# Optimization experiments

Measured on AMD Instinct MI355X. Metric: run time of the kernel, lower is better.

The kernel has to match this reference:

```python
import jax, jax.numpy as jnp
import numpy as np

NPOINT, RADIUS, NSAMPLE = 512, 0.2, 32
MLP = [64, 64, 128]
IN_CH = 67
EPS = 1e-5


def farthest_point_sample(xyz, npoint):
    # xyz: [B, N, 3] -> idx [B, npoint]. Deterministic start at index 0.
    B, N, _ = xyz.shape

    def step(carry, _):
        dist, far = carry  # dist [B,N], far [B]
        centroid = jnp.take_along_axis(xyz, far[:, None, None], axis=1)  # [B,1,3]
        d = jnp.sum((xyz - centroid) ** 2, axis=-1)  # [B,N]
        dist = jnp.minimum(dist, d)
        return (dist, jnp.argmax(dist, axis=-1).astype(jnp.int32)), far

    init = (jnp.full((B, N), 1e10, dtype=xyz.dtype), jnp.zeros((B,), jnp.int32))
    _, idxs = jax.lax.scan(step, init, None, length=npoint)
    return idxs.T  # [B, npoint]


def query_ball_point(radius, nsample, xyz, new_xyz):
    # xyz [B,N,3], new_xyz [B,S,3] -> idx [B,S,nsample]
    B, N, _ = xyz.shape
    sqr = jnp.sum((new_xyz[:, :, None, :] - xyz[:, None, :, :]) ** 2, axis=-1)  # [B,S,N]
    gidx = jnp.where(sqr > radius * radius, N, jnp.arange(N, dtype=jnp.int32))
    gidx = jnp.sort(gidx, axis=-1)[:, :, :nsample]
    first = gidx[:, :, :1]
    return jnp.where(gidx == N, first, gidx).astype(jnp.int32)


def gather_points(pts, idx):
    # pts [B,N,C], idx [B,...] -> [B,...,C]
    return jax.vmap(lambda p, i: p[i])(pts, idx)


def sample_and_group(npoint, radius, nsample, xyz, points):
    fps_idx = farthest_point_sample(xyz, npoint)          # [B,S]
    new_xyz = gather_points(xyz, fps_idx)                 # [B,S,3]
    idx = query_ball_point(radius, nsample, xyz, new_xyz)  # [B,S,K]
    grouped_xyz = gather_points(xyz, idx)                 # [B,S,K,3]
    grouped_xyz_norm = grouped_xyz - new_xyz[:, :, None, :]
    grouped_pts = gather_points(points, idx)              # [B,S,K,D]
    new_points = jnp.concatenate([grouped_xyz_norm, grouped_pts], axis=-1)  # [B,S,K,3+D]
    return new_xyz, new_points


def mlp_bn_relu(x, w, b, gamma, beta):
    # x [B,C,K,S]; 1x1 conv + training-mode BatchNorm2d + ReLU
    y = jnp.einsum('oc,bcks->boks', w, x) + b[None, :, None, None]
    mean = jnp.mean(y, axis=(0, 2, 3), keepdims=True)
    var = jnp.var(y, axis=(0, 2, 3), keepdims=True)
    y = (y - mean) * jax.lax.rsqrt(var + EPS)
    y = y * gamma[None, :, None, None] + beta[None, :, None, None]
    return jax.nn.relu(y)


def setup_inputs() -> dict:
    key = jax.random.key(0)
    ks = jax.random.split(key, 8)
    B, N, D = 16, 2048, 64
    inp = {
        'xyz': jax.random.normal(ks[0], (B, 3, N), jnp.float32),
        'points': jax.random.normal(ks[1], (B, D, N), jnp.float32),
    }
    last = IN_CH
    for i, out in enumerate(MLP):
        kw = jax.random.fold_in(ks[2], i)
        inp[f'w{i}'] = jax.random.normal(kw, (out, last), jnp.float32) * 0.05
        inp[f'b{i}'] = jnp.zeros((out,), jnp.float32)
        inp[f'g{i}'] = jnp.ones((out,), jnp.float32)
        inp[f'bt{i}'] = jnp.zeros((out,), jnp.float32)
        last = out
    return inp


def reference(xyz, points, w0, b0, g0, bt0, w1, b1, g1, bt1, w2, b2, g2, bt2):
    # xyz [B,3,N], points [B,D,N]
    xyz_t = jnp.transpose(xyz, (0, 2, 1))      # [B,N,3]
    pts_t = jnp.transpose(points, (0, 2, 1))   # [B,N,D]
    new_xyz, new_points = sample_and_group(NPOINT, RADIUS, NSAMPLE, xyz_t, pts_t)
    # [B,S,K,C] -> [B,C,K,S]
    x = jnp.transpose(new_points, (0, 3, 2, 1))
    for (w, b, g, bt) in ((w0, b0, g0, bt0), (w1, b1, g1, bt1), (w2, b2, g2, bt2)):
        x = mlp_bn_relu(x, w, b, g, bt)
    feature = jnp.max(x, axis=2)               # [B,C',S]
    new_xyz_out = jnp.transpose(new_xyz, (0, 2, 1))  # [B,3,S]
    return new_xyz_out, feature
```

## Files before the change

kernel.cpp:

```cpp
#include <hip/hip_runtime.h>
#include <hip/hip_bf16.h>
#include <stdint.h>

#define NB 16
#define NPT 2048
#define NS 512
#define NK 32
#define PTOT (NB*NS*NK)
#define C_IN 67
#define EPSV 1e-5f

typedef __attribute__((ext_vector_type(8))) short short8;
typedef __attribute__((ext_vector_type(4))) float floatx4;

#define WS_NEWXYZ 0
#define WS_ST     24576
#define WS_W1BF   27136
#define WS_W2BF   29184
#define WS_RAWMAX 33280
#define WS_PTS_TB 557568
#define WS_Y1     1606144
#define WS_Y2     9994752

__device__ __forceinline__ float bf2f(ushort u){ return __uint_as_float((uint32_t)u<<16); }
__device__ __forceinline__ ushort f2bf(float f){
  uint32_t u = __float_as_uint(f);
  return (ushort)((u + 0x7FFFu + ((u>>16)&1u)) >> 16);
}

template<int CTRL>
__device__ __forceinline__ double dppmax64f(double k){
  long long b = __double_as_longlong(k);
  int lo = (int)(uint32_t)b, hi = (int)(b>>32);
  int olo = __builtin_amdgcn_update_dpp(lo, lo, CTRL, 0xF, 0xF, false);
  int ohi = __builtin_amdgcn_update_dpp(hi, hi, CTRL, 0xF, 0xF, false);
  double o = __hiloint2double(ohi, olo);
  return fmax(o, k);
}
__device__ __forceinline__ unsigned long long u64max(unsigned long long a, unsigned long long b){ return a>b?a:b; }

__global__ __launch_bounds__(256) void prep_kernel(const float* __restrict__ xyz,
    float* __restrict__ nxyz, float* __restrict__ out0,
    const float* __restrict__ pts, ushort* __restrict__ pts_tb,
    const float* __restrict__ w1, const float* __restrict__ w2,
    ushort* __restrict__ w1b, ushort* __restrict__ w2b, float* __restrict__ st)
{
  __shared__ union {
    struct { float4 lc[NPT]; double warr[2][4]; int sel[NS]; } f;
    float tile[64][65];
  } sm;
  const int blk = blockIdx.x;
  const int tid = threadIdx.x;
  if (blk < 16){
    const int b = blk;
    const float* xb = xyz + (size_t)b*3*NPT;
    float px[8], py[8], pz[8], dist[8];
    uint32_t lo_[8];
    #pragma unroll
    for (int j=0;j<8;j++){
      int n = j*256 + tid;
      float x = xb[n], y = xb[NPT+n], z = xb[2*NPT+n];
      sm.f.lc[n] = make_float4(x,y,z,0.f);
      px[j]=x; py[j]=y; pz[j]=z; dist[j]=1e10f;
      lo_[j] = ~(uint32_t)n;
    }
    if (tid==0) sm.f.sel[0]=0;
    __syncthreads();
    float4 c0 = sm.f.lc[0];
    float cx = c0.x, cy = c0.y, cz = c0.z;
    const int lane = tid & 63, wid = tid >> 6;
    for (int t=1;t<NS;t++){
      double kk[8];
      #pragma unroll
      for (int j=0;j<8;j++){
        float dx = __fsub_rn(px[j], cx);
        float dy = __fsub_rn(py[j], cy);
        float dz = __fsub_rn(pz[j], cz);
        float d  = __fadd_rn(__fadd_rn(__fmul_rn(dx,dx),__fmul_rn(dy,dy)),__fmul_rn(dz,dz));
        float dd = fminf(dist[j], d);
        dist[j] = dd;
        kk[j] = __hiloint2double((int)__float_as_uint(dd), (int)lo_[j]);
      }
      double m0 = fmax(kk[0],kk[1]), m1 = fmax(kk[2],kk[3]);
      double m2 = fmax(kk[4],kk[5]), m3 = fmax(kk[6],kk[7]);
      double best = fmax(fmax(m0,m1), fmax(m2,m3));
      best = dppmax64f<0xB1>(best);
      best = dppmax64f<0x4E>(best);
      best = dppmax64f<0x124>(best);
      best = dppmax64f<0x128>(best);
      long long bb = __double_as_longlong(best);
      int bl = (int)(uint32_t)bb, bh = (int)(bb>>32);
      unsigned long long k0 = (((unsigned long long)(uint32_t)__builtin_amdgcn_readlane(bh, 0))<<32)  | (uint32_t)__builtin_amdgcn_readlane(bl, 0);
      unsigned long long k1 = (((unsigned long long)(uint32_t)__builtin_amdgcn_readlane(bh, 16))<<32) | (uint32_t)__builtin_amdgcn_readlane(bl, 16);
      unsigned long long k2 = (((unsigned long long)(uint32_t)__builtin_amdgcn_readlane(bh, 32))<<32) | (uint32_t)__builtin_amdgcn_readlane(bl, 32);
      unsigned long long k3 = (((unsigned long long)(uint32_t)__builtin_amdgcn_readlane(bh, 48))<<32) | (uint32_t)__builtin_amdgcn_readlane(bl, 48);
      unsigned long long kw = u64max(u64max(k0,k1), u64max(k2,k3));
      if (lane==0) sm.f.warr[t&1][wid] = __longlong_as_double((long long)kw);
      __syncthreads();
      double w0 = sm.f.warr[t&1][0], w1_ = sm.f.warr[t&1][1], w2_ = sm.f.warr[t&1][2], w3 = sm.f.warr[t&1][3];
      double f = fmax(fmax(w0,w1_), fmax(w2_,w3));
      int n = (int)(~(uint32_t)__double_as_longlong(f));
      float4 cc = sm.f.lc[n];
      cx = cc.x; cy = cc.y; cz = cc.z;
      if (tid==0) sm.f.sel[t]=n;
    }
    __syncthreads();
    for (int s = tid; s < NS; s += 256){
      int n = sm.f.sel[s];
      float4 cc = sm.f.lc[n];
      float* np_ = nxyz + ((size_t)b*NS + s)*3;
      np_[0]=cc.x; np_[1]=cc.y; np_[2]=cc.z;
      float* ob = out0 + (size_t)b*3*NS + s;
      ob[0]=cc.x; ob[NS]=cc.y; ob[2*NS]=cc.z;
    }
  } else if (blk < 528){
    const int t2 = blk - 16;
    const int b = t2 >> 5;
    const int n0 = (t2 & 31) * 64;
    const int lane = tid & 63;
    const int row4 = tid >> 6;
    const float* src = pts + (size_t)b*64*NPT;
    #pragma unroll
    for (int r=0; r<16; r++){
      int cc = r*4 + row4;
      sm.tile[cc][lane] = src[(size_t)cc*NPT + n0 + lane];
    }
    __syncthreads();
    ushort* dst = pts_tb + ((size_t)b*NPT + n0)*64;
    #pragma unroll
    for (int r=0; r<16; r++){
      int nn = r*4 + row4;
      dst[(size_t)nn*64 + lane] = f2bf(sm.tile[lane][nn]);
    }
  } else {
    for (int i = tid; i < 4096; i += 256) w1b[i] = f2bf(w1[i]);
    for (int i = tid; i < 8192; i += 256) w2b[i] = f2bf(w2[i]);
    for (int i = tid; i < 2560; i += 256) st[i] = 0.f;
  }
}

__global__ __launch_bounds__(256) void conv1_kernel(const float* __restrict__ xyz,
    const ushort* __restrict__ pts_tb, const float* __restrict__ nxyz,
    const float* __restrict__ Wt, const float* __restrict__ bias,
    ushort* __restrict__ y1)
{
  __shared__ int gq[8][NK];
  const int tid = threadIdx.x;
  const int wid = tid>>6, lane = tid&63;
  const int p0 = blockIdx.x*256;
  const int bs0 = p0 >> 5;
  const int b = p0 >> 14;
  const float* xb = xyz + (size_t)b*3*NPT;
  const float r2 = 0.2f*0.2f;
  for (int gi=0; gi<2; gi++){
    const int gl = wid*2 + gi;
    const float* c = nxyz + (size_t)(bs0+gl)*3;
    const float cx = c[0], cy = c[1], cz = c[2];
    int cnt = 0, first = 0;
    for (int ch=0; ch<NPT/64 && cnt<NK; ch++){
      int n = ch*64 + lane;
      float dx = __fsub_rn(cx, xb[n]);
      float dy = __fsub_rn(cy, xb[NPT+n]);
      float dz = __fsub_rn(cz, xb[2*NPT+n]);
      float d  = __fadd_rn(__fadd_rn(__fmul_rn(dx,dx),__fmul_rn(dy,dy)),__fmul_rn(dz,dz));
      bool in = (d <= r2);
      unsigned long long mask = __ballot(in);
      if (mask){
        if (cnt==0) first = ch*64 + (__ffsll((unsigned long long)mask)-1);
        if (in){
          int pos = cnt + __popcll(mask & ((1ull<<lane)-1ull));
          if (pos < NK) gq[gl][pos] = n;
        }
        cnt += __popcll(mask);
      }
    }
    if (cnt < NK && lane >= cnt && lane < NK) gq[gl][lane] = first;
  }
  __syncthreads();
  const int p = p0 + tid;
  const int bs = p >> 5;
  const int n = gq[tid>>5][tid&31];
  float x[C_IN];
  {
    const float* cc = nxyz + (size_t)bs*3;
    x[0] = xb[n]        - cc[0];
    x[1] = xb[NPT+n]    - cc[1];
    x[2] = xb[2*NPT+n]  - cc[2];
    const ushort* pr = pts_tb + ((size_t)b*NPT + n)*64;
    #pragma unroll
    for (int q=0;q<8;q++){
      short8 v = *(const short8*)(pr + q*8);
      #pragma unroll
      for (int j=0;j<8;j++) x[3+8*q+j] = bf2f((ushort)v[j]);
    }
  }
  ushort* yr = y1 + (size_t)p*64;
  #pragma unroll 1
  for (int o=0;o<64;o+=8){
    float a[8];
    #pragma unroll
    for (int k=0;k<8;k++) a[k] = bias[o+k];
    #pragma unroll
    for (int c=0;c<C_IN;c++){
      float xv = x[c];
      #pragma unroll
      for (int k=0;k<8;k++) a[k] = fmaf(Wt[(o+k)*C_IN+c], xv, a[k]);
    }
    short8 sv;
    #pragma unroll
    for (int k=0;k<8;k++) sv[k] = (short)f2bf(a[k]);
    *(short8*)(yr + o) = sv;
  }
}

__global__ __launch_bounds__(256) void stats64_kernel(const ushort* __restrict__ y,
                                                      float* __restrict__ stbase)
{
  const int wid = threadIdx.x>>6, lane = threadIdx.x&63;
  const int oct = lane & 7, pr = lane >> 3;
  const int p0 = blockIdx.x*1024 + wid*256;
  float s[8], s2[8];
  #pragma unroll
  for (int j=0;j<8;j++){ s[j]=0.f; s2[j]=0.f; }
  for (int it=0; it<32; it++){
    int p = p0 + it*8 + pr;
    short8 v = *(const short8*)(y + (size_t)p*64 + oct*8);
    #pragma unroll
    for (int j=0;j<8;j++){
      float f = bf2f((ushort)v[j]);
      s[j] += f; s2[j] = fmaf(f,f,s2[j]);
    }
  }
  #pragma unroll
  for (int off=8; off<64; off<<=1){
    #pragma unroll
    for (int j=0;j<8;j++){ s[j] += __shfl_xor(s[j],off,64); s2[j] += __shfl_xor(s2[j],off,64); }
  }
  __shared__ float sd[4][128];
  if (pr==0){
    #pragma unroll
    for (int j=0;j<8;j++){ sd[wid][oct*8+j] = s[j]; sd[wid][64+oct*8+j] = s2[j]; }
  }
  __syncthreads();
  int t = threadIdx.x;
  if (t < 128){
    float v = sd[0][t]+sd[1][t]+sd[2][t]+sd[3][t];
    int rep = blockIdx.x & 1;
    float* dst = (t<64) ? (stbase + rep*64 + t) : (stbase + 128 + rep*64 + (t-64));
    atomicAdd(dst, v);
  }
}

__global__ __launch_bounds__(256) void conv2_mfma(const ushort* __restrict__ yin,
    const float* __restrict__ st, const float* __restrict__ g0, const float* __restrict__ bt0,
    const ushort* __restrict__ Wb, const float* __restrict__ bias,
    ushort* __restrict__ yout)
{
  __shared__ float aAl[64], aBl[64];
  const int tid = threadIdx.x;
  if (tid < 64){
    float s = st[tid] + st[64+tid];
    float qv = st[128+tid] + st[192+tid];
    float mean = s * (1.f/PTOT);
    float var  = qv * (1.f/PTOT) - mean*mean;
    float a = g0[tid] * rsqrtf(var + EPSV);
    aAl[tid] = a;
    aBl[tid] = fmaf(-mean, a, bt0[tid]);
  }
  __syncthreads();
  const int wid = tid>>6, lane = tid&63;
  const int q = lane>>4, nn = lane&15;
  const int p0 = (blockIdx.x*4 + wid) * 32;
  float a_[2][8], b_[2][8];
  #pragma unroll
  for (int kh=0;kh<2;kh++)
    #pragma unroll
    for (int j=0;j<8;j++){
      a_[kh][j] = aAl[kh*32 + q*8 + j];
      b_[kh][j] = aBl[kh*32 + q*8 + j];
    }
  short8 Af[4][2];
  #pragma unroll
  for (int mt=0;mt<4;mt++)
    #pragma unroll
    for (int kh=0;kh<2;kh++)
      Af[mt][kh] = *(const short8*)(Wb + (mt*16 + nn)*64 + kh*32 + q*8);
  float bias_[4][4];
  #pragma unroll
  for (int mt=0;mt<4;mt++)
    #pragma unroll
    for (int r=0;r<4;r++) bias_[mt][r] = bias[mt*16 + q*4 + r];
  floatx4 z = {0.f,0.f,0.f,0.f};
  floatx4 acc[4][2];
  #pragma unroll
  for (int mt=0;mt<4;mt++){ acc[mt][0]=z; acc[mt][1]=z; }
  #pragma unroll
  for (int nt=0;nt<2;nt++){
    #pragma unroll
    for (int kh=0;kh<2;kh++){
      short8 raw = *(const short8*)(yin + (size_t)(p0 + nt*16 + nn)*64 + kh*32 + q*8);
      short8 bf;
      #pragma unroll
      for (int j=0;j<8;j++){
        float f = bf2f((ushort)raw[j]);
        f = fmaxf(fmaf(f, a_[kh][j], b_[kh][j]), 0.f);
        bf[j] = (short)f2bf(f);
      }
      #pragma unroll
      for (int mt=0;mt<4;mt++)
        acc[mt][nt] = __builtin_amdgcn_mfma_f32_16x16x32_bf16(Af[mt][kh], bf, acc[mt][nt], 0,0,0);
    }
  }
  #pragma unroll
  for (int nt=0;nt<2;nt++){
    int p = p0 + nt*16 + nn;
    #pragma unroll
    for (int mt=0;mt<4;mt++){
      float v0 = acc[mt][nt][0] + bias_[mt][0];
      float v1 = acc[mt][nt][1] + bias_[mt][1];
      float v2 = acc[mt][nt][2] + bias_[mt][2];
      float v3 = acc[mt][nt][3] + bias_[mt][3];
      uint2 w;
      w.x = (uint32_t)f2bf(v0) | ((uint32_t)f2bf(v1)<<16);
      w.y = (uint32_t)f2bf(v2) | ((uint32_t)f2bf(v3)<<16);
      *(uint2*)(yout + (size_t)p*64 + mt*16 + q*4) = w;
    }
  }
}

__global__ __launch_bounds__(256) void conv3_mfma(const ushort* __restrict__ yin,
    float* __restrict__ st, const float* __restrict__ g1, const float* __restrict__ bt1,
    const ushort* __restrict__ Wb, const float* __restrict__ bias,
    ushort* __restrict__ rawmax)
{
  __shared__ ushort tile[64*132];
  __shared__ float aAl[64], aBl[64];
  const int tid = threadIdx.x;
  if (tid < 64){
    float s = st[256+tid] + st[320+tid];
    float qv = st[384+tid] + st[448+tid];
    float mean = s * (1.f/PTOT);
    float var  = qv * (1.f/PTOT) - mean*mean;
    float a = g1[tid] * rsqrtf(var + EPSV);
    aAl[tid] = a;
    aBl[tid] = fmaf(-mean, a, bt1[tid]);
  }
  __syncthreads();
  const int wid = tid>>6, lane = tid&63;
  const int q = lane>>4, nn = lane&15;
  const int p0 = (blockIdx.x*4 + wid) * 16;
  float a_[2][8], b_[2][8];
  #pragma unroll
  for (int kh=0;kh<2;kh++)
    #pragma unroll
    for (int j=0;j<8;j++){
      a_[kh][j] = aAl[kh*32 + q*8 + j];
      b_[kh][j] = aBl[kh*32 + q*8 + j];
    }
  short8 bfr[2];
  #pragma unroll
  for (int kh=0;kh<2;kh++){
    short8 raw = *(const short8*)(yin + (size_t)(p0 + nn)*64 + kh*32 + q*8);
    short8 bf;
    #pragma unroll
    for (int j=0;j<8;j++){
      float f = bf2f((ushort)raw[j]);
      f = fmaxf(fmaf(f, a_[kh][j], b_[kh][j]), 0.f);
      bf[j] = (short)f2bf(f);
    }
    bfr[kh] = bf;
  }
  #pragma unroll 1
  for (int mh=0;mh<2;mh++){
    floatx4 z = {0.f,0.f,0.f,0.f};
    floatx4 acc[4];
    short8 Af[4][2];
    #pragma unroll
    for (int mt=0;mt<4;mt++){
      acc[mt]=z;
      #pragma unroll
      for (int kh=0;kh<2;kh++)
        Af[mt][kh] = *(const short8*)(Wb + ((mh*4+mt)*16 + nn)*64 + kh*32 + q*8);
    }
    #pragma unroll
    for (int kh=0;kh<2;kh++)
      #pragma unroll
      for (int mt=0;mt<4;mt++)
        acc[mt] = __builtin_amdgcn_mfma_f32_16x16x32_bf16(Af[mt][kh], bfr[kh], acc[mt], 0,0,0);
    #pragma unroll
    for (int mt=0;mt<4;mt++){
      int m0 = (mh*4+mt)*16;
      float v0 = acc[mt][0] + bias[m0 + q*4 + 0];
      float v1 = acc[mt][1] + bias[m0 + q*4 + 1];
      float v2 = acc[mt][2] + bias[m0 + q*4 + 2];
      float v3 = acc[mt][3] + bias[m0 + q*4 + 3];
      uint2 w;
      w.x = (uint32_t)f2bf(v0) | ((uint32_t)f2bf(v1)<<16);
      w.y = (uint32_t)f2bf(v2) | ((uint32_t)f2bf(v3)<<16);
      *(uint2*)&tile[(wid*16 + nn)*132 + m0 + q*4] = w;
    }
  }
  __syncthreads();
  const int c = tid >> 1, half = tid & 1;
  float s = 0.f, q2 = 0.f, mx = -1e30f;
  #pragma unroll 4
  for (int it=0; it<32; it++){
    float f = bf2f(tile[(half*32 + it)*132 + c]);
    s += f; q2 = fmaf(f,f,q2); mx = fmaxf(mx, f);
  }
  rawmax[(size_t)(blockIdx.x*2 + half)*128 + c] = f2bf(mx);
  s  += __shfl_xor(s, 1, 64);
  q2 += __shfl_xor(q2, 1, 64);
  if (half==0){
    int rep = blockIdx.x & 7;
    atomicAdd(&st[512  + rep*128 + c], s);
    atomicAdd(&st[1536 + rep*128 + c], q2);
  }
}

__global__ __launch_bounds__(256) void finalize_kernel(const ushort* __restrict__ rawmax,
    const float* __restrict__ st, const float* __restrict__ g2, const float* __restrict__ bt2,
    float* __restrict__ out)
{
  __shared__ float tile[64][65];
  __shared__ float aAl[128], aBl[128];
  const int tid = threadIdx.x;
  if (tid < 128){
    float s=0.f, qv=0.f;
    #pragma unroll
    for (int r=0;r<8;r++){ s += st[512 + r*128 + tid]; qv += st[1536 + r*128 + tid]; }
    float mean = s * (1.f/PTOT);
    float var  = qv * (1.f/PTOT) - mean*mean;
    float a = g2[tid] * rsqrtf(var + EPSV);
    aAl[tid] = a;
    aBl[tid] = fmaf(-mean, a, bt2[tid]);
  }
  __syncthreads();
  const int b  = blockIdx.x >> 4;
  const int ct = (blockIdx.x >> 3) & 1;
  const int stt = blockIdx.x & 7;
  const int c0 = ct*64, s0 = stt*64;
  const int lane = tid & 63, wid = tid >> 6;
  #pragma unroll
  for (int r=0;r<16;r++){
    int sl = r*4 + wid;
    tile[sl][lane] = bf2f(rawmax[((size_t)(b*512 + s0 + sl))*128 + c0 + lane]);
  }
  __syncthreads();
  #pragma unroll
  for (int r=0;r<16;r++){
    int cl = r*4 + wid;
    float a = aAl[c0+cl], bb = aBl[c0+cl];
    out[((size_t)(b*128 + c0 + cl))*512 + s0 + lane] = fmaxf(fmaf(tile[lane][cl], a, bb), 0.f);
  }
}

extern "C" void kernel_launch(void* const* d_in, const int* in_sizes, int n_in,
                              void* d_out, int out_size, void* d_ws, size_t ws_size,
                              hipStream_t stream) {
  const float* xyz = (const float*)d_in[0];
  const float* pts = (const float*)d_in[1];
  const float* w0  = (const float*)d_in[2];
  const float* b0  = (const float*)d_in[3];
  const float* g0  = (const float*)d_in[4];
  const float* bt0 = (const float*)d_in[5];
  const float* w1  = (const float*)d_in[6];
  const float* b1  = (const float*)d_in[7];
  const float* g1  = (const float*)d_in[8];
  const float* bt1 = (const float*)d_in[9];
  const float* w2  = (const float*)d_in[10];
  const float* b2  = (const float*)d_in[11];
  const float* g2  = (const float*)d_in[12];
  const float* bt2 = (const float*)d_in[13];
  float* out = (float*)d_out;
  float* ws  = (float*)d_ws;

  float* nxyz = ws + WS_NEWXYZ;
  float* st   = ws + WS_ST;
  ushort* w1b = (ushort*)(ws + WS_W1BF);
  ushort* w2b = (ushort*)(ws + WS_W2BF);
  ushort* rawmax = (ushort*)(ws + WS_RAWMAX);
  ushort* pts_tb = (ushort*)(ws + WS_PTS_TB);
  ushort* y1 = (ushort*)(ws + WS_Y1);
  ushort* y2 = (ushort*)(ws + WS_Y2);

  prep_kernel<<<529,256,0,stream>>>(xyz, nxyz, out, pts, pts_tb, w1, w2, w1b, w2b, st);
  conv1_kernel<<<PTOT/256,256,0,stream>>>(xyz, pts_tb, nxyz, w0, b0, y1);
  stats64_kernel<<<256,256,0,stream>>>(y1, st);
  conv2_mfma<<<2048,256,0,stream>>>(y1, st, g0, bt0, w1b, b1, y2);
  stats64_kernel<<<256,256,0,stream>>>(y2, st + 256);
  conv3_mfma<<<4096,256,0,stream>>>(y2, st, g1, bt1, w2b, b2, rawmax);
  finalize_kernel<<<256,256,0,stream>>>(rawmax, st, g2, bt2, out + NB*3*NS);
}
```

Before: 510.7 us.

## Move first conv layer onto bf16 MFMA and streamline FPS argmax reduction

Replaces the scalar per-point FMA loop of the first 1x1 conv with a bf16 MFMA kernel, one wave per centroid group. The weights are reordered and padded to K=96 in the prep kernel, with the xyz offsets fed as an extra K block. Separately, the farthest-point-sampling loop now finishes the wave reduction with row broadcasts and a single readlane. It also passes the winning coordinates through shared memory, so no dependent index lookup is needed after the barrier. Costs include bf16 rounding of the xyz offsets and padded MFMA work on the extra K block.

```diff
diff --git a/kernel.cpp b/kernel.cpp
--- a/kernel.cpp
+++ b/kernel.cpp
@@ -7,7 +7,6 @@
 #define NS 512
 #define NK 32
 #define PTOT (NB*NS*NK)
-#define C_IN 67
 #define EPSV 1e-5f
 
 typedef __attribute__((ext_vector_type(8))) short short8;
@@ -17,10 +16,11 @@
 #define WS_ST     24576
 #define WS_W1BF   27136
 #define WS_W2BF   29184
-#define WS_RAWMAX 33280
-#define WS_PTS_TB 557568
-#define WS_Y1     1606144
-#define WS_Y2     9994752
+#define WS_W0R    33280
+#define WS_RAWMAX 36352
+#define WS_PTS_TB 560640
+#define WS_Y1     1609216
+#define WS_Y2     9997824
 
 __device__ __forceinline__ float bf2f(ushort u){ return __uint_as_float((uint32_t)u<<16); }
 __device__ __forceinline__ ushort f2bf(float f){
@@ -37,16 +37,16 @@
   double o = __hiloint2double(ohi, olo);
   return fmax(o, k);
 }
-__device__ __forceinline__ unsigned long long u64max(unsigned long long a, unsigned long long b){ return a>b?a:b; }
 
 __global__ __launch_bounds__(256) void prep_kernel(const float* __restrict__ xyz,
     float* __restrict__ nxyz, float* __restrict__ out0,
     const float* __restrict__ pts, ushort* __restrict__ pts_tb,
-    const float* __restrict__ w1, const float* __restrict__ w2,
-    ushort* __restrict__ w1b, ushort* __restrict__ w2b, float* __restrict__ st)
+    const float* __restrict__ w0, const float* __restrict__ w1, const float* __restrict__ w2,
+    ushort* __restrict__ w0r, ushort* __restrict__ w1b, ushort* __restrict__ w2b,
+    float* __restrict__ st)
 {
   __shared__ union {
-    struct { float4 lc[NPT]; double warr[2][4]; int sel[NS]; } f;
+    struct { float4 lc[NPT]; double warrK[2][4]; float4 warrC[2][4]; float4 csel[NS]; } f;
     float tile[64][65];
   } sm;
   const int blk = blockIdx.x;
@@ -64,10 +64,10 @@
       px[j]=x; py[j]=y; pz[j]=z; dist[j]=1e10f;
       lo_[j] = ~(uint32_t)n;
     }
-    if (tid==0) sm.f.sel[0]=0;
     __syncthreads();
     float4 c0 = sm.f.lc[0];
     float cx = c0.x, cy = c0.y, cz = c0.z;
+    if (tid==0) sm.f.csel[0] = make_float4(cx,cy,cz,0.f);
     const int lane = tid & 63, wid = tid >> 6;
     for (int t=1;t<NS;t++){
       double kk[8];
@@ -88,26 +88,33 @@
       best = dppmax64f<0x4E>(best);
       best = dppmax64f<0x124>(best);
       best = dppmax64f<0x128>(best);
+      best = dppmax64f<0x142>(best);
+      best = dppmax64f<0x143>(best);
       long long bb = __double_as_longlong(best);
       int bl = (int)(uint32_t)bb, bh = (int)(bb>>32);
-      unsigned long long k0 = (((unsigned long long)(uint32_t)__builtin_amdgcn_readlane(bh, 0))<<32)  | (uint32_t)__builtin_amdgcn_readlane(bl, 0);
-      unsigned long long k1 = (((unsigned long long)(uint32_t)__builtin_amdgcn_readlane(bh, 16))<<32) | (uint32_t)__builtin_amdgcn_readlane(bl, 16);
-      unsigned long long k2 = (((unsigned long long)(uint32_t)__builtin_amdgcn_readlane(bh, 32))<<32) | (uint32_t)__builtin_amdgcn_readlane(bl, 32);
-      unsigned long long k3 = (((unsigned long long)(uint32_t)__builtin_amdgcn_readlane(bh, 48))<<32) | (uint32_t)__builtin_amdgcn_readlane(bl, 48);
-      unsigned long long kw = u64max(u64max(k0,k1), u64max(k2,k3));
-      if (lane==0) sm.f.warr[t&1][wid] = __longlong_as_double((long long)kw);
+      uint32_t lo63 = (uint32_t)__builtin_amdgcn_readlane(bl, 63);
+      uint32_t hi63 = (uint32_t)__builtin_amdgcn_readlane(bh, 63);
+      int n_w = (int)(~lo63);
+      float4 cw = sm.f.lc[n_w];
+      const int tb = t & 1;
+      if (lane==0){
+        sm.f.warrK[tb][wid] = __hiloint2double((int)hi63, (int)lo63);
+        sm.f.warrC[tb][wid] = cw;
+      }
       __syncthreads();
-      double w0 = sm.f.warr[t&1][0], w1_ = sm.f.warr[t&1][1], w2_ = sm.f.warr[t&1][2], w3 = sm.f.warr[t&1][3];
-      double f = fmax(fmax(w0,w1_), fmax(w2_,w3));
-      int n = (int)(~(uint32_t)__double_as_longlong(f));
-      float4 cc = sm.f.lc[n];
-      cx = cc.x; cy = cc.y; cz = cc.z;
-      if (tid==0) sm.f.sel[t]=n;
+      double k0 = sm.f.warrK[tb][0], k1 = sm.f.warrK[tb][1];
+      double k2 = sm.f.warrK[tb][2], k3 = sm.f.warrK[tb][3];
+      float4 cc0 = sm.f.warrC[tb][0], cc1 = sm.f.warrC[tb][1];
+      float4 cc2 = sm.f.warrC[tb][2], cc3 = sm.f.warrC[tb][3];
+      if (k1 > k0){ k0 = k1; cc0 = cc1; }
+      if (k3 > k2){ k2 = k3; cc2 = cc3; }
+      if (k2 > k0){ k0 = k2; cc0 = cc2; }
+      cx = cc0.x; cy = cc0.y; cz = cc0.z;
+      if (tid==0) sm.f.csel[t] = make_float4(cx,cy,cz,0.f);
     }
     __syncthreads();
     for (int s = tid; s < NS; s += 256){
-      int n = sm.f.sel[s];
-      float4 cc = sm.f.lc[n];
+      float4 cc = sm.f.csel[s];
       float* np_ = nxyz + ((size_t)b*NS + s)*3;
       np_[0]=cc.x; np_[1]=cc.y; np_[2]=cc.z;
       float* ob = out0 + (size_t)b*3*NS + s;
@@ -136,26 +143,30 @@
     for (int i = tid; i < 4096; i += 256) w1b[i] = f2bf(w1[i]);
     for (int i = tid; i < 8192; i += 256) w2b[i] = f2bf(w2[i]);
     for (int i = tid; i < 2560; i += 256) st[i] = 0.f;
-  }
-}
-
-__global__ __launch_bounds__(256) void conv1_kernel(const float* __restrict__ xyz,
+    for (int i = tid; i < 6144; i += 256){
+      int o = i / 96, k = i - o*96;
+      float v = (k < 64) ? w0[o*67 + 3 + k] : ((k < 67) ? w0[o*67 + (k-64)] : 0.f);
+      w0r[i] = f2bf(v);
+    }
+  }
+}
+
+__global__ __launch_bounds__(256) void conv1_mfma(const float* __restrict__ xyz,
     const ushort* __restrict__ pts_tb, const float* __restrict__ nxyz,
-    const float* __restrict__ Wt, const float* __restrict__ bias,
+    const ushort* __restrict__ w0r, const float* __restrict__ b0,
     ushort* __restrict__ y1)
 {
-  __shared__ int gq[8][NK];
+  __shared__ int gq[4][NK];
   const int tid = threadIdx.x;
   const int wid = tid>>6, lane = tid&63;
-  const int p0 = blockIdx.x*256;
-  const int bs0 = p0 >> 5;
-  const int b = p0 >> 14;
+  const int q = lane>>4, nn = lane&15;
+  const int g = blockIdx.x*4 + wid;
+  const int b = g >> 9;
   const float* xb = xyz + (size_t)b*3*NPT;
-  const float r2 = 0.2f*0.2f;
-  for (int gi=0; gi<2; gi++){
-    const int gl = wid*2 + gi;
-    const float* c = nxyz + (size_t)(bs0+gl)*3;
-    const float cx = c[0], cy = c[1], cz = c[2];
+  const float* cgp = nxyz + (size_t)g*3;
+  const float cx = cgp[0], cy = cgp[1], cz = cgp[2];
+  {
+    const float r2 = 0.2f*0.2f;
     int cnt = 0, first = 0;
     for (int ch=0; ch<NPT/64 && cnt<NK; ch++){
       int n = ch*64 + lane;
@@ -169,47 +180,65 @@
         if (cnt==0) first = ch*64 + (__ffsll((unsigned long long)mask)-1);
         if (in){
           int pos = cnt + __popcll(mask & ((1ull<<lane)-1ull));
-          if (pos < NK) gq[gl][pos] = n;
+          if (pos < NK) gq[wid][pos] = n;
         }
         cnt += __popcll(mask);
       }
     }
-    if (cnt < NK && lane >= cnt && lane < NK) gq[gl][lane] = first;
-  }
-  __syncthreads();
-  const int p = p0 + tid;
-  const int bs = p >> 5;
-  const int n = gq[tid>>5][tid&31];
-  float x[C_IN];
+    if (cnt < NK && lane >= cnt && lane < NK) gq[wid][lane] = first;
+  }
+  int n0 = gq[wid][nn], n1 = gq[wid][16+nn];
+  float dx0 = xb[n0]-cx, dy0 = xb[NPT+n0]-cy, dz0 = xb[2*NPT+n0]-cz;
+  float dx1 = xb[n1]-cx, dy1 = xb[NPT+n1]-cy, dz1 = xb[2*NPT+n1]-cz;
+  floatx4 z4 = {0.f,0.f,0.f,0.f};
+  floatx4 acc[4][2];
+  #pragma unroll
+  for (int mt=0;mt<4;mt++){ acc[mt][0]=z4; acc[mt][1]=z4; }
+  const ushort* pr0 = pts_tb + ((size_t)b*NPT + n0)*64;
+  const ushort* pr1 = pts_tb + ((size_t)b*NPT + n1)*64;
+  #pragma unroll
+  for (int kh=0; kh<2; kh++){
+    short8 B0 = *(const short8*)(pr0 + kh*32 + q*8);
+    short8 B1 = *(const short8*)(pr1 + kh*32 + q*8);
+    #pragma unroll
+    for (int mt=0; mt<4; mt++){
+      short8 A = *(const short8*)(w0r + (mt*16+nn)*96 + kh*32 + q*8);
+      acc[mt][0] = __builtin_amdgcn_mfma_f32_16x16x32_bf16(A, B0, acc[mt][0], 0,0,0);
+      acc[mt][1] = __builtin_amdgcn_mfma_f32_16x16x32_bf16(A, B1, acc[mt][1], 0,0,0);
+    }
+  }
   {
-    const float* cc = nxyz + (size_t)bs*3;
-    x[0] = xb[n]        - cc[0];
-    x[1] = xb[NPT+n]    - cc[1];
-    x[2] = xb[2*NPT+n]  - cc[2];
-    const ushort* pr = pts_tb + ((size_t)b*NPT + n)*64;
-    #pragma unroll
-    for (int q=0;q<8;q++){
-      short8 v = *(const short8*)(pr + q*8);
-      #pragma unroll
-      for (int j=0;j<8;j++) x[3+8*q+j] = bf2f((ushort)v[j]);
-    }
-  }
-  ushort* yr = y1 + (size_t)p*64;
-  #pragma unroll 1
-  for (int o=0;o<64;o+=8){
-    float a[8];
-    #pragma unroll
-    for (int k=0;k<8;k++) a[k] = bias[o+k];
-    #pragma unroll
-    for (int c=0;c<C_IN;c++){
-      float xv = x[c];
-      #pragma unroll
-      for (int k=0;k<8;k++) a[k] = fmaf(Wt[(o+k)*C_IN+c], xv, a[k]);
-    }
-    short8 sv;
-    #pragma unroll
-    for (int k=0;k<8;k++) sv[k] = (short)f2bf(a[k]);
-    *(short8*)(yr + o) = sv;
+    short8 B0 = {0,0,0,0,0,0,0,0}, B1 = {0,0,0,0,0,0,0,0};
+    if (q==0){
+      B0[0]=(short)f2bf(dx0); B0[1]=(short)f2bf(dy0); B0[2]=(short)f2bf(dz0);
+      B1[0]=(short)f2bf(dx1); B1[1]=(short)f2bf(dy1); B1[2]=(short)f2bf(dz1);
+    }
+    #pragma unroll
+    for (int mt=0; mt<4; mt++){
+      short8 A = *(const short8*)(w0r + (mt*16+nn)*96 + 64 + q*8);
+      acc[mt][0] = __builtin_amdgcn_mfma_f32_16x16x32_bf16(A, B0, acc[mt][0], 0,0,0);
+      acc[mt][1] = __builtin_amdgcn_mfma_f32_16x16x32_bf16(A, B1, acc[mt][1], 0,0,0);
+    }
+  }
+  float bias_[4][4];
+  #pragma unroll
+  for (int mt=0;mt<4;mt++)
+    #pragma unroll
+    for (int r=0;r<4;r++) bias_[mt][r] = b0[mt*16 + q*4 + r];
+  #pragma unroll
+  for (int nt=0; nt<2; nt++){
+    int p = g*32 + nt*16 + nn;
+    #pragma unroll
+    for (int mt=0; mt<4; mt++){
+      float v0 = acc[mt][nt][0] + bias_[mt][0];
+      float v1 = acc[mt][nt][1] + bias_[mt][1];
+      float v2 = acc[mt][nt][2] + bias_[mt][2];
+      float v3 = acc[mt][nt][3] + bias_[mt][3];
+      uint2 wv;
+      wv.x = (uint32_t)f2bf(v0) | ((uint32_t)f2bf(v1)<<16);
+      wv.y = (uint32_t)f2bf(v2) | ((uint32_t)f2bf(v3)<<16);
+      *(uint2*)(y1 + (size_t)p*64 + mt*16 + q*4) = wv;
+    }
   }
 }
 
@@ -477,6 +506,7 @@
 
   float* nxyz = ws + WS_NEWXYZ;
   float* st   = ws + WS_ST;
+  ushort* w0r = (ushort*)(ws + WS_W0R);
   ushort* w1b = (ushort*)(ws + WS_W1BF);
   ushort* w2b = (ushort*)(ws + WS_W2BF);
   ushort* rawmax = (ushort*)(ws + WS_RAWMAX);
@@ -484,8 +514,8 @@
   ushort* y1 = (ushort*)(ws + WS_Y1);
   ushort* y2 = (ushort*)(ws + WS_Y2);
 
-  prep_kernel<<<529,256,0,stream>>>(xyz, nxyz, out, pts, pts_tb, w1, w2, w1b, w2b, st);
-  conv1_kernel<<<PTOT/256,256,0,stream>>>(xyz, pts_tb, nxyz, w0, b0, y1);
+  prep_kernel<<<529,256,0,stream>>>(xyz, nxyz, out, pts, pts_tb, w0, w1, w2, w0r, w1b, w2b, st);
+  conv1_mfma<<<2048,256,0,stream>>>(xyz, pts_tb, nxyz, w0r, b0, y1);
   stats64_kernel<<<256,256,0,stream>>>(y1, st);
   conv2_mfma<<<2048,256,0,stream>>>(y1, st, g0, bt0, w1b, b1, y2);
   stats64_kernel<<<256,256,0,stream>>>(y2, st + 256);
```

After: 447.6 us. 12.3% less time.
